# Kernel optimization log

Measured on AMD Instinct MI355X. Metric: run time of the kernel, lower is better.

## Reference

```python
import jax, jax.numpy as jnp
import numpy as np

N_HEAD = 16
N_EMBD = 1024
BLOCK = 2048
B, T = 4, 2048


def setup_inputs() -> dict:
    key = jax.random.key(0)
    ks = jax.random.split(key, 5)
    s = 0.02
    return {
        "x": jax.random.normal(ks[0], (B, T, N_EMBD), dtype=jnp.float32),
        "qkv_w": jax.random.normal(ks[1], (3 * N_EMBD, N_EMBD), dtype=jnp.float32) * s,
        "qkv_b": jnp.zeros((3 * N_EMBD,), dtype=jnp.float32),
        "proj_w": jax.random.normal(ks[2], (N_EMBD, N_EMBD), dtype=jnp.float32) * s,
        "proj_b": jnp.zeros((N_EMBD,), dtype=jnp.float32),
    }


def reference(x, qkv_w, qkv_b, proj_w, proj_b):
    Bx, Tx, C = x.shape
    hd = C // N_HEAD
    qkv = x @ qkv_w.T + qkv_b  # [B,T,3C]
    q, k, v = jnp.split(qkv, 3, axis=-1)
    # [B,T,C] -> [B,H,T,hd]
    def heads(t):
        return t.reshape(Bx, Tx, N_HEAD, hd).transpose(0, 2, 1, 3)
    q, k, v = heads(q), heads(k), heads(v)
    scores = jnp.einsum("bhqd,bhkd->bhqk", q, k) / jnp.sqrt(jnp.float32(hd))
    causal = jnp.tril(jnp.ones((Tx, Tx), dtype=bool))
    scores = jnp.where(causal[None, None, :, :], scores, -jnp.inf)
    attn = jax.nn.softmax(scores, axis=-1)
    out = jnp.einsum("bhqk,bhkd->bhqd", attn, v)
    out = out.transpose(0, 2, 1, 3).reshape(Bx, Tx, C)
    return out @ proj_w.T + proj_b
```

## Files before the change

kernel.cpp:

```cpp
#include <hip/hip_runtime.h>
#include <stdint.h>
#include <math.h>

#define DEVI __device__ __forceinline__

typedef __attribute__((ext_vector_type(8))) short bf16x8;
typedef __attribute__((ext_vector_type(4))) float f32x4;

DEVI unsigned short f2bf(float f) {
  union { float f; unsigned u; } v; v.f = f;
  unsigned u = v.u;
  u += 0x7fffu + ((u >> 16) & 1u);
  return (unsigned short)(u >> 16);
}

DEVI unsigned cvt_pk_bf16(float a, float b) {
  unsigned r;
  asm("v_cvt_pk_bf16_f32 %0, %1, %2" : "=v"(r) : "v"(a), "v"(b));
  return r;
}

DEVI f32x4 mfma16(bf16x8 a, bf16x8 b, f32x4 c) {
  return __builtin_amdgcn_mfma_f32_16x16x32_bf16(a, b, c, 0, 0, 0);
}

DEVI void gld16(const unsigned short* g, unsigned short* l) {
  __builtin_amdgcn_global_load_lds(
      (const __attribute__((address_space(1))) unsigned int*)(uintptr_t)g,
      (__attribute__((address_space(3))) unsigned int*)(unsigned int)(uintptr_t)l,
      16, 0, 0);
}

__global__ __launch_bounds__(256) void cvt_kernel(const float* __restrict__ in,
                                                  unsigned short* __restrict__ out, int n) {
  int i = (blockIdx.x * 256 + threadIdx.x) * 4;
  if (i < n) {
    float4 v = *(const float4*)(in + i);
    unsigned lo = f2bf(v.x) | ((unsigned)f2bf(v.y) << 16);
    unsigned hi = f2bf(v.z) | ((unsigned)f2bf(v.w) << 16);
    uint2 o; o.x = lo; o.y = hi;
    *(uint2*)(out + i) = o;
  }
}

template <int MODE>
__global__ __launch_bounds__(256) void gemm_bt(
    const unsigned short* __restrict__ A, const unsigned short* __restrict__ Bw,
    const float* __restrict__ bias, float* __restrict__ Cf,
    unsigned short* __restrict__ Qo, unsigned short* __restrict__ Ko,
    unsigned short* __restrict__ Vo, int M, int N, int K) {
  __shared__ unsigned short As[128 * 64];
  __shared__ unsigned short Bs[128 * 64];
  const int tid = threadIdx.x;
  const int lane = tid & 63;
  const int w = tid >> 6;
  const int wm = w & 1, wn = w >> 1;
  const int lr = lane & 15, lq = lane >> 4;
  const int m0 = blockIdx.y * 128;
  const int n0 = blockIdx.x * 128;
  const int l8r = lane >> 3;
  const int l8c = (lane & 7) << 3;

  f32x4 acc[4][4] = {};

  for (int kt = 0; kt < K; kt += 64) {
    __syncthreads();
#pragma unroll
    for (int i = 0; i < 4; ++i) {
      int c = w * 4 + i;
      int row = c * 8 + l8r;
      gld16(A + (size_t)(m0 + row) * K + kt + l8c, &As[c * 8 * 64]);
      gld16(Bw + (size_t)(n0 + row) * K + kt + l8c, &Bs[c * 8 * 64]);
    }
    __syncthreads();
#pragma unroll
    for (int kk = 0; kk < 64; kk += 32) {
      bf16x8 af[4], bfr[4];
#pragma unroll
      for (int mt = 0; mt < 4; ++mt)
        af[mt] = *(const bf16x8*)(&As[(wm * 64 + mt * 16 + lr) * 64 + kk + lq * 8]);
#pragma unroll
      for (int nt = 0; nt < 4; ++nt)
        bfr[nt] = *(const bf16x8*)(&Bs[(wn * 64 + nt * 16 + lr) * 64 + kk + lq * 8]);
#pragma unroll
      for (int mt = 0; mt < 4; ++mt)
#pragma unroll
        for (int nt = 0; nt < 4; ++nt)
          acc[mt][nt] = mfma16(af[mt], bfr[nt], acc[mt][nt]);
    }
  }

#pragma unroll
  for (int mt = 0; mt < 4; ++mt) {
#pragma unroll
    for (int nt = 0; nt < 4; ++nt) {
      int n_g = n0 + wn * 64 + nt * 16 + lr;
      float bv = bias[n_g];
#pragma unroll
      for (int r = 0; r < 4; ++r) {
        int m_g = m0 + wm * 64 + mt * 16 + lq * 4 + r;
        float v = acc[mt][nt][r] + bv;
        if (MODE == 1) {
          Cf[(size_t)m_g * N + n_g] = v;
        } else {
          int which = n_g >> 10;
          int rem = n_g & 1023;
          int h = rem >> 6, d = rem & 63;
          int b = m_g >> 11, t = m_g & 2047;
          size_t idx = (((size_t)(b * 16 + h) * 2048) + t) * 64 + d;
          unsigned short* p = (which == 0) ? Qo : ((which == 1) ? Ko : Vo);
          p[idx] = f2bf(v);
        }
      }
    }
  }
}

__global__ __launch_bounds__(512, 4) void attn_kernel(
    const unsigned short* __restrict__ Q, const unsigned short* __restrict__ K,
    const unsigned short* __restrict__ V, unsigned short* __restrict__ Y) {
  constexpr int T = 2048, HD = 64, H = 16;
  __shared__ unsigned short Kt[2][64 * 72];
  __shared__ unsigned short Vt[2][64 * 72];
  __shared__ unsigned short Pt[8][16 * 72];

  const int tid = threadIdx.x;
  const int lane = tid & 63;
  const int w = tid >> 6;
  const int lr = lane & 15, lq = lane >> 4;
  const int pair = blockIdx.x;
  const int h = blockIdx.y;
  const int b = blockIdx.z;
  const size_t bh = (size_t)(b * H + h) * T * HD;
  const float SC = 0.125f * 1.44269504089f;

  const int krow = tid >> 3, kcb = (tid & 7) << 3;
  const int vrow = lane, vc = w << 3;

  float4 kr, vr;
  auto load_tile = [&](int jt) {
    const int c0 = jt * 64;
    kr = *(const float4*)(K + bh + (size_t)(c0 + krow) * HD + kcb);
    vr = *(const float4*)(V + bh + (size_t)(c0 + vrow) * HD + vc);
  };
  auto stage = [&](int buf) {
    *(float4*)(&Kt[buf][krow * 72 + kcb]) = kr;
    const unsigned short* vp = (const unsigned short*)&vr;
#pragma unroll
    for (int j = 0; j < 8; ++j) Vt[buf][(vc + j) * 72 + vrow] = vp[j];
  };

  load_tile(0);

  for (int phase = 0; phase < 2; ++phase) {
    const int qt = phase ? (15 - pair) : pair;
    const int q0 = qt * 128;
    const int nkv = 2 * qt + 2;
    const int qmin = q0 + w * 16;
    const int qmax = qmin + 15;

    bf16x8 qf[2];
#pragma unroll
    for (int kb = 0; kb < 2; ++kb)
      qf[kb] = *(const bf16x8*)(Q + bh + (size_t)(qmin + lr) * HD + kb * 32 + lq * 8);

    f32x4 o[4] = {};
    float mi = -INFINITY, li = 0.f;

    stage(0);
    load_tile(1);
    __syncthreads();

    for (int jt = 0; jt < nkv; ++jt) {
      const int c0 = jt * 64;
      const int buf = jt & 1;

      if (c0 <= qmax) {
        f32x4 s[4];
#pragma unroll
        for (int nt = 0; nt < 4; ++nt) {
          bf16x8 kf0 = *(const bf16x8*)(&Kt[buf][(nt * 16 + lr) * 72 + lq * 8]);
          bf16x8 kf1 = *(const bf16x8*)(&Kt[buf][(nt * 16 + lr) * 72 + 32 + lq * 8]);
          f32x4 z = {};
          z = mfma16(kf0, qf[0], z);
          s[nt] = mfma16(kf1, qf[1], z);
        }
        if (c0 + 63 > qmin) {
          int qg = qmin + lr;
#pragma unroll
          for (int nt = 0; nt < 4; ++nt)
#pragma unroll
            for (int r = 0; r < 4; ++r) {
              int kvg = c0 + nt * 16 + lq * 4 + r;
              s[nt][r] = (kvg > qg) ? -INFINITY : s[nt][r] * SC;
            }
        } else {
#pragma unroll
          for (int nt = 0; nt < 4; ++nt)
#pragma unroll
            for (int r = 0; r < 4; ++r) s[nt][r] *= SC;
        }
        float mx = -INFINITY;
#pragma unroll
        for (int nt = 0; nt < 4; ++nt)
          mx = fmaxf(mx, fmaxf(fmaxf(s[nt][0], s[nt][1]),
                               fmaxf(s[nt][2], s[nt][3])));
        mx = fmaxf(mx, __shfl_xor(mx, 16));
        mx = fmaxf(mx, __shfl_xor(mx, 32));
        float mnew = fmaxf(mi, mx);
        float alpha = __builtin_amdgcn_exp2f(mi - mnew);
        mi = mnew;
        float rs = 0.f;
#pragma unroll
        for (int nt = 0; nt < 4; ++nt) {
          float p0 = __builtin_amdgcn_exp2f(s[nt][0] - mnew);
          float p1 = __builtin_amdgcn_exp2f(s[nt][1] - mnew);
          float p2 = __builtin_amdgcn_exp2f(s[nt][2] - mnew);
          float p3 = __builtin_amdgcn_exp2f(s[nt][3] - mnew);
          rs += (p0 + p1) + (p2 + p3);
          uint2 pk;
          pk.x = cvt_pk_bf16(p0, p1);
          pk.y = cvt_pk_bf16(p2, p3);
          *(uint2*)(&Pt[w][lr * 72 + nt * 16 + lq * 4]) = pk;
        }
        rs += __shfl_xor(rs, 16);
        rs += __shfl_xor(rs, 32);
        li = li * alpha + rs;
#pragma unroll
        for (int nt = 0; nt < 4; ++nt)
#pragma unroll
          for (int r = 0; r < 4; ++r) o[nt][r] *= alpha;
        bf16x8 pf[2];
#pragma unroll
        for (int kb = 0; kb < 2; ++kb)
          pf[kb] = *(const bf16x8*)(&Pt[w][lr * 72 + kb * 32 + lq * 8]);
#pragma unroll
        for (int nt = 0; nt < 4; ++nt) {
          bf16x8 vf0 = *(const bf16x8*)(&Vt[buf][(nt * 16 + lr) * 72 + lq * 8]);
          bf16x8 vf1 = *(const bf16x8*)(&Vt[buf][(nt * 16 + lr) * 72 + 32 + lq * 8]);
          o[nt] = mfma16(vf0, pf[0], o[nt]);
          o[nt] = mfma16(vf1, pf[1], o[nt]);
        }
      }

      if (jt + 1 < nkv) {
        stage(buf ^ 1);
        if (jt + 2 < nkv) load_tile(jt + 2);
        else if (phase == 0) load_tile(0);
        __syncthreads();
      }
    }

    {
      float inv = 1.f / li;
      int t_g = qmin + lr;
#pragma unroll
      for (int nt = 0; nt < 4; ++nt) {
        uint2 yv;
        yv.x = cvt_pk_bf16(o[nt][0] * inv, o[nt][1] * inv);
        yv.y = cvt_pk_bf16(o[nt][2] * inv, o[nt][3] * inv);
        *(uint2*)(Y + ((size_t)(b * T + t_g)) * 1024 + h * 64 + nt * 16 + lq * 4) = yv;
      }
    }
  }
}

extern "C" void kernel_launch(void* const* d_in, const int* in_sizes, int n_in,
                              void* d_out, int out_size, void* d_ws, size_t ws_size,
                              hipStream_t stream) {
  const float* x = (const float*)d_in[0];
  const float* qkv_w = (const float*)d_in[1];
  const float* qkv_b = (const float*)d_in[2];
  const float* proj_w = (const float*)d_in[3];
  const float* proj_b = (const float*)d_in[4];
  float* out = (float*)d_out;

  unsigned short* ws = (unsigned short*)d_ws;
  unsigned short* xb = ws;
  unsigned short* wqkv = xb + 8388608;
  unsigned short* wproj = wqkv + 3145728;
  unsigned short* Qb = wproj + 1048576;
  unsigned short* Kb = Qb + 8388608;
  unsigned short* Vb = Kb + 8388608;
  unsigned short* Yb = Vb + 8388608;

  cvt_kernel<<<8388608 / 1024, 256, 0, stream>>>(x, xb, 8388608);
  cvt_kernel<<<3145728 / 1024, 256, 0, stream>>>(qkv_w, wqkv, 3145728);
  cvt_kernel<<<1048576 / 1024, 256, 0, stream>>>(proj_w, wproj, 1048576);

  gemm_bt<0><<<dim3(24, 64), 256, 0, stream>>>(xb, wqkv, qkv_b, nullptr, Qb, Kb, Vb,
                                               8192, 3072, 1024);
  attn_kernel<<<dim3(8, 16, 4), 512, 0, stream>>>(Qb, Kb, Vb, Yb);
  gemm_bt<1><<<dim3(8, 64), 256, 0, stream>>>(Yb, wproj, proj_b, out, nullptr, nullptr,
                                              nullptr, 8192, 1024, 1024);
}
```

Measured before the change: 278.2 us.

## Rewrite GEMMs as 256x256 double-buffered 8-wave kernel with swizzled LDS

Replaces the 128x128 4-wave GEMM with a 256x256 tile, 8-wave kernel that double-buffers 128 KB of dynamic LDS, interleaving async global-to-LDS loads for the next K tile with MFMA phases under explicit vmcnt waits and barriers. LDS columns are XOR-swizzled to avoid bank conflicts, block IDs are remapped for cache locality, and MFMA sections are raised in priority. This aims to hide load latency and raise arithmetic intensity, at the cost of more registers, fragile hand-tuned wait counts, and fewer blocks for the small projection GEMM (128 blocks).

```diff
diff --git a/kernel.cpp b/kernel.cpp
--- a/kernel.cpp
+++ b/kernel.cpp
@@ -30,6 +30,13 @@
       (__attribute__((address_space(3))) unsigned int*)(unsigned int)(uintptr_t)l,
       16, 0, 0);
 }
+
+#define VMCNT(n) asm volatile("s_waitcnt vmcnt(" #n ")" ::: "memory")
+#define BAR()                              \
+  do {                                     \
+    __builtin_amdgcn_s_barrier();          \
+    __builtin_amdgcn_sched_barrier(0);     \
+  } while (0)
 
 __global__ __launch_bounds__(256) void cvt_kernel(const float* __restrict__ in,
                                                   unsigned short* __restrict__ out, int n) {
@@ -44,61 +51,114 @@
 }
 
 template <int MODE>
-__global__ __launch_bounds__(256) void gemm_bt(
+__global__ __launch_bounds__(512, 2) void gemm8(
     const unsigned short* __restrict__ A, const unsigned short* __restrict__ Bw,
     const float* __restrict__ bias, float* __restrict__ Cf,
     unsigned short* __restrict__ Qo, unsigned short* __restrict__ Ko,
-    unsigned short* __restrict__ Vo, int M, int N, int K) {
-  __shared__ unsigned short As[128 * 64];
-  __shared__ unsigned short Bs[128 * 64];
+    unsigned short* __restrict__ Vo, int M, int N, int K, int nbx) {
+  extern __shared__ unsigned short lds[];
   const int tid = threadIdx.x;
   const int lane = tid & 63;
   const int w = tid >> 6;
-  const int wm = w & 1, wn = w >> 1;
+  const int wm = w >> 2, wn = w & 3;
   const int lr = lane & 15, lq = lane >> 4;
-  const int m0 = blockIdx.y * 128;
-  const int n0 = blockIdx.x * 128;
-  const int l8r = lane >> 3;
-  const int l8c = (lane & 7) << 3;
-
-  f32x4 acc[4][4] = {};
-
-  for (int kt = 0; kt < K; kt += 64) {
-    __syncthreads();
-#pragma unroll
-    for (int i = 0; i < 4; ++i) {
-      int c = w * 4 + i;
-      int row = c * 8 + l8r;
-      gld16(A + (size_t)(m0 + row) * K + kt + l8c, &As[c * 8 * 64]);
-      gld16(Bw + (size_t)(n0 + row) * K + kt + l8c, &Bs[c * 8 * 64]);
-    }
-    __syncthreads();
-#pragma unroll
-    for (int kk = 0; kk < 64; kk += 32) {
-      bf16x8 af[4], bfr[4];
-#pragma unroll
-      for (int mt = 0; mt < 4; ++mt)
-        af[mt] = *(const bf16x8*)(&As[(wm * 64 + mt * 16 + lr) * 64 + kk + lq * 8]);
-#pragma unroll
-      for (int nt = 0; nt < 4; ++nt)
-        bfr[nt] = *(const bf16x8*)(&Bs[(wn * 64 + nt * 16 + lr) * 64 + kk + lq * 8]);
-#pragma unroll
-      for (int mt = 0; mt < 4; ++mt)
-#pragma unroll
-        for (int nt = 0; nt < 4; ++nt)
-          acc[mt][nt] = mfma16(af[mt], bfr[nt], acc[mt][nt]);
-    }
-  }
-
-#pragma unroll
-  for (int mt = 0; mt < 4; ++mt) {
+
+  const int cpx = gridDim.x >> 3;
+  const int swz = (blockIdx.x & 7) * cpx + (blockIdx.x >> 3);
+  const int bx = swz % nbx, by = swz / nbx;
+  const int m0 = by * 256, n0 = bx * 256;
+
+  const int sr = lane >> 3;
+  const int sc = ((lane & 7) ^ sr) << 3;
+  const unsigned short* pa = A + (size_t)(m0 + sr) * K + sc;
+  const unsigned short* pb = Bw + (size_t)(n0 + sr) * K + sc;
+
+  const int aA0 = w, aA1 = 16 + w;
+  const int aB0 = 8 + w, aB1 = 24 + w;
+  const int bA0 = (w & 3) + ((w >> 2) << 3), bA1 = bA0 + 16;
+  const int bB0 = bA0 + 4, bB1 = bA1 + 4;
+
+  const int bs0 = (lq ^ (lr & 7)) << 3;
+  const int bs1 = ((lq + 4) ^ (lr & 7)) << 3;
+
+  f32x4 acc[8][4] = {};
+
+  auto sA = [&](int buf, int kt, int c) {
+    gld16(pa + (size_t)(c << 3) * K + kt, lds + buf * 32768 + (c << 9));
+  };
+  auto sB = [&](int buf, int kt, int c) {
+    gld16(pb + (size_t)(c << 3) * K + kt, lds + buf * 32768 + 16384 + (c << 9));
+  };
+
+#define PH(buf, mh, nh)                                                          \
+  {                                                                              \
+    const unsigned short* As_ = lds + (buf) * 32768;                             \
+    const unsigned short* Bs_ = As_ + 16384;                                     \
+    bf16x8 a0[4], a1[4], b0[2], b1[2];                                           \
+    _Pragma("unroll") for (int i = 0; i < 4; ++i) {                              \
+      int ar = wm * 128 + (mh) * 64 + i * 16 + lr;                               \
+      a0[i] = *(const bf16x8*)(As_ + ar * 64 + bs0);                             \
+      a1[i] = *(const bf16x8*)(As_ + ar * 64 + bs1);                             \
+    }                                                                            \
+    _Pragma("unroll") for (int j = 0; j < 2; ++j) {                              \
+      int br = wn * 64 + (nh) * 32 + j * 16 + lr;                                \
+      b0[j] = *(const bf16x8*)(Bs_ + br * 64 + bs0);                             \
+      b1[j] = *(const bf16x8*)(Bs_ + br * 64 + bs1);                             \
+    }                                                                            \
+    __builtin_amdgcn_s_setprio(1);                                               \
+    _Pragma("unroll") for (int i = 0; i < 4; ++i)                                \
+      _Pragma("unroll") for (int j = 0; j < 2; ++j) {                            \
+        acc[(mh) * 4 + i][(nh) * 2 + j] =                                        \
+            mfma16(a0[i], b0[j], acc[(mh) * 4 + i][(nh) * 2 + j]);               \
+        acc[(mh) * 4 + i][(nh) * 2 + j] =                                        \
+            mfma16(a1[i], b1[j], acc[(mh) * 4 + i][(nh) * 2 + j]);               \
+      }                                                                          \
+    __builtin_amdgcn_s_setprio(0);                                               \
+  }
+
+  sA(0, 0, aA0); sA(0, 0, aA1);
+  sB(0, 0, bA0); sB(0, 0, bA1);
+  sB(0, 0, bB0); sB(0, 0, bB1);
+  sA(0, 0, aB0); sA(0, 0, aB1);
+  VMCNT(4);
+  BAR();
+
+  const int NT = K >> 6;
+  for (int t = 0; t < NT - 1; ++t) {
+    const int buf = t & 1, nb = buf ^ 1;
+    const int kt = (t + 1) << 6;
+    sA(nb, kt, aA0); sA(nb, kt, aA1);
+    PH(buf, 0, 0);
+    VMCNT(4); BAR();
+    sB(nb, kt, bA0); sB(nb, kt, bA1);
+    PH(buf, 0, 1);
+    VMCNT(4); BAR();
+    sB(nb, kt, bB0); sB(nb, kt, bB1);
+    PH(buf, 1, 0);
+    sA(nb, kt, aB0); sA(nb, kt, aB1);
+    PH(buf, 1, 1);
+    VMCNT(4); BAR();
+  }
+  {
+    const int buf = (NT - 1) & 1;
+    PH(buf, 0, 0);
+    VMCNT(2); BAR();
+    PH(buf, 0, 1);
+    VMCNT(0); BAR();
+    PH(buf, 1, 0);
+    PH(buf, 1, 1);
+  }
+#undef PH
+
+#pragma unroll
+  for (int mt = 0; mt < 8; ++mt) {
 #pragma unroll
     for (int nt = 0; nt < 4; ++nt) {
       int n_g = n0 + wn * 64 + nt * 16 + lr;
       float bv = bias[n_g];
 #pragma unroll
       for (int r = 0; r < 4; ++r) {
-        int m_g = m0 + wm * 64 + mt * 16 + lq * 4 + r;
+        int m_g = m0 + wm * 128 + mt * 16 + lq * 4 + r;
         float v = acc[mt][nt][r] + bv;
         if (MODE == 1) {
           Cf[(size_t)m_g * N + n_g] = v;
@@ -106,8 +166,8 @@
           int which = n_g >> 10;
           int rem = n_g & 1023;
           int h = rem >> 6, d = rem & 63;
-          int b = m_g >> 11, t = m_g & 2047;
-          size_t idx = (((size_t)(b * 16 + h) * 2048) + t) * 64 + d;
+          int b = m_g >> 11, tt = m_g & 2047;
+          size_t idx = (((size_t)(b * 16 + h) * 2048) + tt) * 64 + d;
           unsigned short* p = (which == 0) ? Qo : ((which == 1) ? Ko : Vo);
           p[idx] = f2bf(v);
         }
@@ -284,13 +344,24 @@
   unsigned short* Vb = Kb + 8388608;
   unsigned short* Yb = Vb + 8388608;
 
+  auto* g0 = gemm8<0>;
+  auto* g1 = gemm8<1>;
+  static bool attr_set = false;
+  if (!attr_set) {
+    (void)hipFuncSetAttribute((const void*)g0,
+                              hipFuncAttributeMaxDynamicSharedMemorySize, 131072);
+    (void)hipFuncSetAttribute((const void*)g1,
+                              hipFuncAttributeMaxDynamicSharedMemorySize, 131072);
+    attr_set = true;
+  }
+
   cvt_kernel<<<8388608 / 1024, 256, 0, stream>>>(x, xb, 8388608);
   cvt_kernel<<<3145728 / 1024, 256, 0, stream>>>(qkv_w, wqkv, 3145728);
   cvt_kernel<<<1048576 / 1024, 256, 0, stream>>>(proj_w, wproj, 1048576);
 
-  gemm_bt<0><<<dim3(24, 64), 256, 0, stream>>>(xb, wqkv, qkv_b, nullptr, Qb, Kb, Vb,
-                                               8192, 3072, 1024);
+  gemm8<0><<<dim3(384), 512, 131072, stream>>>(xb, wqkv, qkv_b, nullptr, Qb, Kb, Vb,
+                                               8192, 3072, 1024, 12);
   attn_kernel<<<dim3(8, 16, 4), 512, 0, stream>>>(Qb, Kb, Vb, Yb);
-  gemm_bt<1><<<dim3(8, 64), 256, 0, stream>>>(Yb, wproj, proj_b, out, nullptr, nullptr,
-                                              nullptr, 8192, 1024, 1024);
-}
+  gemm8<1><<<dim3(128), 512, 131072, stream>>>(Yb, wproj, proj_b, out, nullptr, nullptr,
+                                               nullptr, 8192, 1024, 1024, 4);
+}
```

Measured after the change: 261.4 us. 6.0% less time.
